# Performance work log

Hardware: AMD Instinct MI355X
Metric: run time of the kernel (lower is better)

Reference implementation:

```python
import jax, jax.numpy as jnp
import numpy as np

N = 50000          # num nodes
EPS = 1e-5         # BatchNorm eps


def _spmm(row, col, val, x):
    # sparse (COO) @ dense: out[r] += val_e * x[c] for each edge e=(r,c)
    return jax.ops.segment_sum(val[:, None] * x[col], row, num_segments=N)


def setup_inputs() -> dict:
    key = jax.random.key(0)
    ks = jax.random.split(key, 12)
    E1, E2 = 1_000_000, 2_000_000
    IN, H, OUT = 512, 64, 40
    return {
        "x": jax.random.normal(ks[0], (N, IN), jnp.float32),
        "adj_row": jax.random.randint(ks[1], (E1,), 0, N, jnp.int32),
        "adj_col": jax.random.randint(ks[2], (E1,), 0, N, jnp.int32),
        "adj_val": jax.random.uniform(ks[3], (E1,), jnp.float32),
        "adj2_row": jax.random.randint(ks[4], (E2,), 0, N, jnp.int32),
        "adj2_col": jax.random.randint(ks[5], (E2,), 0, N, jnp.int32),
        "adj2_val": jax.random.uniform(ks[6], (E2,), jnp.float32),
        "W_embed": jax.random.normal(ks[7], (IN, H), jnp.float32) * 0.05,
        "b_embed": jnp.zeros((H,), jnp.float32),
        "bn_gamma": jnp.ones((2 * H,), jnp.float32),
        "bn_beta": jnp.zeros((2 * H,), jnp.float32),
        "bn_mean": jax.random.normal(ks[8], (2 * H,), jnp.float32) * 0.1,
        "bn_var": jax.random.uniform(ks[9], (2 * H,), jnp.float32) + 0.5,
        "W_final": jax.random.normal(ks[10], (7 * H, OUT), jnp.float32) * 0.05,
        "b_final": jnp.zeros((OUT,), jnp.float32),
    }


def reference(x, adj_row, adj_col, adj_val, adj2_row, adj2_col, adj2_val,
              W_embed, b_embed, bn_gamma, bn_beta, bn_mean, bn_var,
              W_final, b_final):
    # feature embed (1-layer MLP) + relu
    h = jax.nn.relu(x @ W_embed + b_embed)                       # [N, H]
    xs = [h]
    # conv 1: two-hop aggregation + concat, then BatchNorm (eval mode)
    h1 = jnp.concatenate([_spmm(adj_row, adj_col, adj_val, h),
                          _spmm(adj2_row, adj2_col, adj2_val, h)], axis=1)  # [N, 2H]
    h1 = (h1 - bn_mean) * jax.lax.rsqrt(bn_var + EPS) * bn_gamma + bn_beta
    xs.append(h1)
    # conv 2 (last conv, no BN)
    h2 = jnp.concatenate([_spmm(adj_row, adj_col, adj_val, h1),
                          _spmm(adj2_row, adj2_col, adj2_val, h1)], axis=1)  # [N, 4H]
    xs.append(h2)
    # JumpingKnowledge cat -> [N, 7H], final projection
    jk = jnp.concatenate(xs, axis=1)
    return jk @ W_final + b_final                                # [N, OUT]
```

## Files before the change

kernel.cpp:

```cpp
#include <hip/hip_runtime.h>

#define BN_EPS 1e-5f
#define MAXBINS 128

typedef __attribute__((ext_vector_type(8))) short bf16x8;
typedef __attribute__((ext_vector_type(4))) float f32x4;

__device__ __forceinline__ ushort f2bf(float f) {
  uint u = __float_as_uint(f);
  u += 0x7fffu + ((u >> 16) & 1u);
  return (ushort)(u >> 16);
}
__device__ __forceinline__ float bf2f(ushort u) {
  return __uint_as_float((uint)u << 16);
}
__device__ __forceinline__ uint pack2bf(float a, float b) {
  return (uint)f2bf(a) | ((uint)f2bf(b) << 16);
}
__device__ __forceinline__ void fma8(float acc[8], uint4 wv, float v) {
  acc[0] += v * __uint_as_float(wv.x << 16);
  acc[1] += v * __uint_as_float(wv.x & 0xffff0000u);
  acc[2] += v * __uint_as_float(wv.y << 16);
  acc[3] += v * __uint_as_float(wv.y & 0xffff0000u);
  acc[4] += v * __uint_as_float(wv.z << 16);
  acc[5] += v * __uint_as_float(wv.z & 0xffff0000u);
  acc[6] += v * __uint_as_float(wv.w << 16);
  acc[7] += v * __uint_as_float(wv.w & 0xffff0000u);
}

__global__ __launch_bounds__(256) void prep_weights(
    const float* __restrict__ We, const float* __restrict__ Wf,
    ushort* __restrict__ Wet, ushort* __restrict__ Wtg) {
  int i = blockIdx.x * 256 + threadIdx.x;
  if (i < 32768) {
    int col = i >> 9, k = i & 511;
    Wet[(size_t)col * 512 + k] = f2bf(We[(size_t)k * 64 + col]);
  } else if (i < 32768 + 24576) {
    int j = i - 32768;
    int col = j / 192, k = j % 192;
    float v = 0.f;
    if (col < 40)       v = Wf[(size_t)k * 40 + col];
    else if (col < 80)  { if (k >= 64) v = Wf[(size_t)(128 + k) * 40 + (col - 40)]; }
    else if (col < 120) { if (k >= 64) v = Wf[(size_t)(256 + k) * 40 + (col - 80)]; }
    Wtg[(size_t)col * 192 + k] = f2bf(v);
  }
}

__global__ __launch_bounds__(256) void embed_mfma(
    const float* __restrict__ x, const ushort* __restrict__ Wet,
    const float* __restrict__ b, ushort* __restrict__ hb, int N) {
  const int tid  = threadIdx.x;
  const int wv   = tid >> 6;
  const int lane = tid & 63;
  const int m16  = lane & 15;
  const int kg   = lane >> 4;
  const int row0 = blockIdx.x * 128 + wv * 32;

  f32x4 acc[2][4];
#pragma unroll
  for (int i = 0; i < 2; ++i)
#pragma unroll
    for (int t = 0; t < 4; ++t) acc[i][t] = (f32x4){0.f, 0.f, 0.f, 0.f};

#pragma unroll 4
  for (int ks = 0; ks < 16; ++ks) {
    const int kk = ks * 32 + kg * 8;
    bf16x8 afr[2];
#pragma unroll
    for (int i = 0; i < 2; ++i) {
      int grow = row0 + i * 16 + m16;
      grow = (grow < N) ? grow : (N - 1);
      const float* ap = x + (size_t)grow * 512 + kk;
      float4 lo = *reinterpret_cast<const float4*>(ap);
      float4 hi = *reinterpret_cast<const float4*>(ap + 4);
      uint4 pk;
      pk.x = pack2bf(lo.x, lo.y); pk.y = pack2bf(lo.z, lo.w);
      pk.z = pack2bf(hi.x, hi.y); pk.w = pack2bf(hi.z, hi.w);
      afr[i] = *reinterpret_cast<const bf16x8*>(&pk);
    }
#pragma unroll
    for (int t = 0; t < 4; ++t) {
      bf16x8 bfr = *reinterpret_cast<const bf16x8*>(
          Wet + (size_t)(t * 16 + m16) * 512 + kk);
      acc[0][t] = __builtin_amdgcn_mfma_f32_16x16x32_bf16(afr[0], bfr, acc[0][t], 0, 0, 0);
      acc[1][t] = __builtin_amdgcn_mfma_f32_16x16x32_bf16(afr[1], bfr, acc[1][t], 0, 0, 0);
    }
  }

#pragma unroll
  for (int i = 0; i < 2; ++i) {
    const int rbase = row0 + i * 16 + kg * 4;
#pragma unroll
    for (int t = 0; t < 4; ++t) {
      const int col = t * 16 + m16;
      const float bias = b[col];
#pragma unroll
      for (int reg = 0; reg < 4; ++reg) {
        int gr = rbase + reg;
        if (gr < N)
          hb[(size_t)gr * 64 + col] = f2bf(fmaxf(acc[i][t][reg] + bias, 0.f));
      }
    }
  }
}

__global__ __launch_bounds__(256) void bin_hist(
    const int* __restrict__ rows, int* __restrict__ gbin, int E, int nbins) {
  __shared__ int lb[MAXBINS];
  const int tid = threadIdx.x;
  if (tid < nbins) lb[tid] = 0;
  __syncthreads();
  const int stride = gridDim.x * blockDim.x;
  for (int i = blockIdx.x * blockDim.x + tid; i < E; i += stride)
    atomicAdd(&lb[rows[i] >> 9], 1);
  __syncthreads();
  if (tid < nbins && lb[tid]) atomicAdd(&gbin[tid], lb[tid]);
}

__device__ __forceinline__ void scan_bins_dev(
    const int* gbin, int* gbase, int* gcur, int nbins, int lane) {
  int carry = 0;
  for (int ch = 0; ch * 64 < nbins; ++ch) {
    int idx = ch * 64 + lane;
    int v = (idx < nbins) ? gbin[idx] : 0;
    int inc = v;
#pragma unroll
    for (int off = 1; off < 64; off <<= 1) {
      int y = __shfl_up(inc, off);
      if (lane >= off) inc += y;
    }
    int ex = carry + inc - v;
    if (idx < nbins) { gbase[idx] = ex; gcur[idx] = ex; }
    carry += __shfl(inc, 63);
  }
}

__global__ __launch_bounds__(64) void bin_scan(
    const int* __restrict__ gbin1, int* __restrict__ gbase1, int* __restrict__ gcur1,
    const int* __restrict__ gbin2, int* __restrict__ gbase2, int* __restrict__ gcur2,
    int nbins) {
  int lane = threadIdx.x;
  scan_bins_dev(gbin1, gbase1, gcur1, nbins, lane);
  scan_bins_dev(gbin2, gbase2, gcur2, nbins, lane);
}

__global__ __launch_bounds__(256) void bin_scatter(
    const int* __restrict__ rows, const int* __restrict__ cols,
    const float* __restrict__ vals, int E, int* __restrict__ gcur,
    int2* __restrict__ S, int nbins) {
  __shared__ int lcnt[MAXBINS];
  __shared__ int lcur[MAXBINS];
  const int tid = threadIdx.x;
  for (int e0 = blockIdx.x * 2048; e0 < E; e0 += gridDim.x * 2048) {
    int i0 = e0 + tid * 8;
    int r[8], c[8], vb[8];
    if (i0 + 8 <= E) {
      int4 a = *reinterpret_cast<const int4*>(rows + i0);
      int4 b = *reinterpret_cast<const int4*>(rows + i0 + 4);
      r[0]=a.x; r[1]=a.y; r[2]=a.z; r[3]=a.w; r[4]=b.x; r[5]=b.y; r[6]=b.z; r[7]=b.w;
      a = *reinterpret_cast<const int4*>(cols + i0);
      b = *reinterpret_cast<const int4*>(cols + i0 + 4);
      c[0]=a.x; c[1]=a.y; c[2]=a.z; c[3]=a.w; c[4]=b.x; c[5]=b.y; c[6]=b.z; c[7]=b.w;
      a = *reinterpret_cast<const int4*>(vals + i0);
      b = *reinterpret_cast<const int4*>(vals + i0 + 4);
      vb[0]=a.x; vb[1]=a.y; vb[2]=a.z; vb[3]=a.w; vb[4]=b.x; vb[5]=b.y; vb[6]=b.z; vb[7]=b.w;
    } else {
#pragma unroll
      for (int t = 0; t < 8; ++t) {
        int i = i0 + t;
        bool ok = i < E;
        r[t]  = ok ? rows[i] : -1;
        c[t]  = ok ? cols[i] : 0;
        vb[t] = ok ? __float_as_int(vals[i]) : 0;
      }
    }
    if (tid < nbins) lcnt[tid] = 0;
    __syncthreads();
#pragma unroll
    for (int t = 0; t < 8; ++t)
      if (r[t] >= 0) atomicAdd(&lcnt[r[t] >> 9], 1);
    __syncthreads();
    if (tid < nbins) {
      int n = lcnt[tid];
      lcur[tid] = n ? atomicAdd(&gcur[tid], n) : 0;
    }
    __syncthreads();
#pragma unroll
    for (int t = 0; t < 8; ++t) {
      if (r[t] >= 0) {
        int pos = atomicAdd(&lcur[r[t] >> 9], 1);
        S[pos] = make_int2(c[t] | ((r[t] & 511) << 16), vb[t]);
      }
    }
    __syncthreads();
  }
}

__global__ __launch_bounds__(256) void csr_finalize(
    const int2* __restrict__ S1, const int* __restrict__ gbase1,
    int* __restrict__ rp1, uint* __restrict__ Eo1, int Etot1,
    const int2* __restrict__ S2, const int* __restrict__ gbase2,
    int* __restrict__ rp2, uint* __restrict__ Eo2, int Etot2,
    int N, int nbins) {
  __shared__ int cnt[512];
  __shared__ int cur[512];
  const int tid = threadIdx.x;
  const int b = blockIdx.x % nbins;
  const int g = blockIdx.x / nbins;
  const int2* S     = g ? S2 : S1;
  const int* gbase  = g ? gbase2 : gbase1;
  int* rp           = g ? rp2 : rp1;
  uint* Eo          = g ? Eo2 : Eo1;
  const int Etot    = g ? Etot2 : Etot1;

  const int base = gbase[b];
  const int end  = (b + 1 < nbins) ? gbase[b + 1] : Etot;
  const int r0   = b << 9;
  const int nrows = min(512, N - r0);

  for (int l = tid; l < 512; l += 256) cnt[l] = 0;
  __syncthreads();
  for (int j = base + tid; j < end; j += 256)
    atomicAdd(&cnt[S[j].x >> 16], 1);
  __syncthreads();
  if (tid < 64) {
    int carry = 0;
#pragma unroll
    for (int ch = 0; ch < 8; ++ch) {
      int v = cnt[ch * 64 + tid];
      int inc = v;
#pragma unroll
      for (int off = 1; off < 64; off <<= 1) {
        int y = __shfl_up(inc, off);
        if (tid >= off) inc += y;
      }
      inc += carry;
      cnt[ch * 64 + tid] = inc;
      carry = __shfl(inc, 63);
    }
  }
  __syncthreads();
  for (int l = tid; l < 512; l += 256)
    cur[l] = base + ((l > 0) ? cnt[l - 1] : 0);
  for (int l = tid; l < nrows; l += 256)
    rp[r0 + l + 1] = base + cnt[l];
  if (b == 0 && tid == 0) rp[0] = 0;
  __syncthreads();
  for (int j = base + tid; j < end; j += 256) {
    int2 m = S[j];
    int pos = atomicAdd(&cur[m.x >> 16], 1);
    Eo[pos] = (uint)(m.x & 0xffff) | ((uint)f2bf(__int_as_float(m.y)) << 16);
  }
}

__global__ __launch_bounds__(256) void conv1_gather(
    const ushort* __restrict__ hb,
    const int* __restrict__ rp1, const uint* __restrict__ E1,
    const int* __restrict__ rp2, const uint* __restrict__ E2,
    const float* __restrict__ gamma, const float* __restrict__ beta,
    const float* __restrict__ mean, const float* __restrict__ var,
    ushort* __restrict__ h1b, int N, int nwaves) {
  const int wid  = (blockIdx.x * blockDim.x + threadIdx.x) >> 6;
  const int lane = threadIdx.x & 63;
  const int sub  = lane >> 3;
  const int q    = lane & 7;

  float sc1[8], sh1[8], sc2[8], sh2[8];
#pragma unroll
  for (int t4 = 0; t4 < 2; ++t4) {
    int f1 = q * 8 + t4 * 4;
    float4 gm = *reinterpret_cast<const float4*>(gamma + f1);
    float4 vr = *reinterpret_cast<const float4*>(var + f1);
    float4 mn = *reinterpret_cast<const float4*>(mean + f1);
    float4 bt = *reinterpret_cast<const float4*>(beta + f1);
    float s0 = gm.x * rsqrtf(vr.x + BN_EPS), s1 = gm.y * rsqrtf(vr.y + BN_EPS);
    float s2 = gm.z * rsqrtf(vr.z + BN_EPS), s3 = gm.w * rsqrtf(vr.w + BN_EPS);
    sc1[t4 * 4 + 0] = s0; sh1[t4 * 4 + 0] = bt.x - mn.x * s0;
    sc1[t4 * 4 + 1] = s1; sh1[t4 * 4 + 1] = bt.y - mn.y * s1;
    sc1[t4 * 4 + 2] = s2; sh1[t4 * 4 + 2] = bt.z - mn.z * s2;
    sc1[t4 * 4 + 3] = s3; sh1[t4 * 4 + 3] = bt.w - mn.w * s3;
    int f2 = 64 + f1;
    gm = *reinterpret_cast<const float4*>(gamma + f2);
    vr = *reinterpret_cast<const float4*>(var + f2);
    mn = *reinterpret_cast<const float4*>(mean + f2);
    bt = *reinterpret_cast<const float4*>(beta + f2);
    s0 = gm.x * rsqrtf(vr.x + BN_EPS); s1 = gm.y * rsqrtf(vr.y + BN_EPS);
    s2 = gm.z * rsqrtf(vr.z + BN_EPS); s3 = gm.w * rsqrtf(vr.w + BN_EPS);
    sc2[t4 * 4 + 0] = s0; sh2[t4 * 4 + 0] = bt.x - mn.x * s0;
    sc2[t4 * 4 + 1] = s1; sh2[t4 * 4 + 1] = bt.y - mn.y * s1;
    sc2[t4 * 4 + 2] = s2; sh2[t4 * 4 + 2] = bt.z - mn.z * s2;
    sc2[t4 * 4 + 3] = s3; sh2[t4 * 4 + 3] = bt.w - mn.w * s3;
  }

  for (int r = wid; r < N; r += nwaves) {
    float acc1[8] = {0, 0, 0, 0, 0, 0, 0, 0};
    float acc2[8] = {0, 0, 0, 0, 0, 0, 0, 0};
    {
      int s = rp1[r], e = rp1[r + 1];
      for (int j0 = s; j0 < e; j0 += 32) {
        int j = j0 + sub;
        uint m0 = (j      < e) ? E1[j]      : 0u;
        uint m1 = (j + 8  < e) ? E1[j + 8]  : 0u;
        uint m2 = (j + 16 < e) ? E1[j + 16] : 0u;
        uint m3 = (j + 24 < e) ? E1[j + 24] : 0u;
        uint4 w0 = *reinterpret_cast<const uint4*>(hb + (size_t)(m0 & 0xffffu) * 64 + q * 8);
        uint4 w1 = *reinterpret_cast<const uint4*>(hb + (size_t)(m1 & 0xffffu) * 64 + q * 8);
        uint4 w2 = *reinterpret_cast<const uint4*>(hb + (size_t)(m2 & 0xffffu) * 64 + q * 8);
        uint4 w3 = *reinterpret_cast<const uint4*>(hb + (size_t)(m3 & 0xffffu) * 64 + q * 8);
        fma8(acc1, w0, bf2f((ushort)(m0 >> 16)));
        fma8(acc1, w1, bf2f((ushort)(m1 >> 16)));
        fma8(acc1, w2, bf2f((ushort)(m2 >> 16)));
        fma8(acc1, w3, bf2f((ushort)(m3 >> 16)));
      }
    }
    {
      int s = rp2[r], e = rp2[r + 1];
      for (int j0 = s; j0 < e; j0 += 32) {
        int j = j0 + sub;
        uint m0 = (j      < e) ? E2[j]      : 0u;
        uint m1 = (j + 8  < e) ? E2[j + 8]  : 0u;
        uint m2 = (j + 16 < e) ? E2[j + 16] : 0u;
        uint m3 = (j + 24 < e) ? E2[j + 24] : 0u;
        uint4 w0 = *reinterpret_cast<const uint4*>(hb + (size_t)(m0 & 0xffffu) * 64 + q * 8);
        uint4 w1 = *reinterpret_cast<const uint4*>(hb + (size_t)(m1 & 0xffffu) * 64 + q * 8);
        uint4 w2 = *reinterpret_cast<const uint4*>(hb + (size_t)(m2 & 0xffffu) * 64 + q * 8);
        uint4 w3 = *reinterpret_cast<const uint4*>(hb + (size_t)(m3 & 0xffffu) * 64 + q * 8);
        fma8(acc2, w0, bf2f((ushort)(m0 >> 16)));
        fma8(acc2, w1, bf2f((ushort)(m1 >> 16)));
        fma8(acc2, w2, bf2f((ushort)(m2 >> 16)));
        fma8(acc2, w3, bf2f((ushort)(m3 >> 16)));
      }
    }
#pragma unroll
    for (int mask = 8; mask <= 32; mask <<= 1) {
#pragma unroll
      for (int t = 0; t < 8; ++t) {
        acc1[t] += __shfl_xor(acc1[t], mask);
        acc2[t] += __shfl_xor(acc2[t], mask);
      }
    }
    if (lane < 8) {
      uint4 p1, p2;
      p1.x = pack2bf(acc1[0] * sc1[0] + sh1[0], acc1[1] * sc1[1] + sh1[1]);
      p1.y = pack2bf(acc1[2] * sc1[2] + sh1[2], acc1[3] * sc1[3] + sh1[3]);
      p1.z = pack2bf(acc1[4] * sc1[4] + sh1[4], acc1[5] * sc1[5] + sh1[5]);
      p1.w = pack2bf(acc1[6] * sc1[6] + sh1[6], acc1[7] * sc1[7] + sh1[7]);
      p2.x = pack2bf(acc2[0] * sc2[0] + sh2[0], acc2[1] * sc2[1] + sh2[1]);
      p2.y = pack2bf(acc2[2] * sc2[2] + sh2[2], acc2[3] * sc2[3] + sh2[3]);
      p2.z = pack2bf(acc2[4] * sc2[4] + sh2[4], acc2[5] * sc2[5] + sh2[5]);
      p2.w = pack2bf(acc2[6] * sc2[6] + sh2[6], acc2[7] * sc2[7] + sh2[7]);
      ushort* dst = h1b + (size_t)r * 128 + q * 8;
      *reinterpret_cast<uint4*>(dst)      = p1;
      *reinterpret_cast<uint4*>(dst + 64) = p2;
    }
  }
}

__global__ __launch_bounds__(256) void dense_tail_mfma(
    const ushort* __restrict__ hb, const ushort* __restrict__ h1b,
    const ushort* __restrict__ Wtg, const float* __restrict__ bfin,
    float* __restrict__ out, ushort* __restrict__ g1b, ushort* __restrict__ g2b,
    int N) {
  const int tid  = threadIdx.x;
  const int wv   = tid >> 6;
  const int lane = tid & 63;
  const int m16  = lane & 15;
  const int kg   = lane >> 4;
  const int row0 = blockIdx.x * 128;

  f32x4 acc[2][8];
#pragma unroll
  for (int i = 0; i < 2; ++i)
#pragma unroll
    for (int t = 0; t < 8; ++t) acc[i][t] = (f32x4){0.f, 0.f, 0.f, 0.f};

#pragma unroll
  for (int ks = 0; ks < 6; ++ks) {
    const int kk = ks * 32 + kg * 8;
    bf16x8 afr[2];
#pragma unroll
    for (int i = 0; i < 2; ++i) {
      int grow = row0 + wv * 32 + i * 16 + m16;
      grow = (grow < N) ? grow : (N - 1);
      const ushort* ap = (kk < 64) ? hb + (size_t)grow * 64 + kk
                                   : h1b + (size_t)grow * 128 + (kk - 64);
      afr[i] = *reinterpret_cast<const bf16x8*>(ap);
    }
#pragma unroll
    for (int t = 0; t < 8; ++t) {
      bf16x8 bfr = *reinterpret_cast<const bf16x8*>(
          Wtg + (size_t)(t * 16 + m16) * 192 + kk);
      acc[0][t] = __builtin_amdgcn_mfma_f32_16x16x32_bf16(afr[0], bfr, acc[0][t], 0, 0, 0);
      acc[1][t] = __builtin_amdgcn_mfma_f32_16x16x32_bf16(afr[1], bfr, acc[1][t], 0, 0, 0);
    }
  }

#pragma unroll
  for (int i = 0; i < 2; ++i) {
    const int rbase = row0 + wv * 32 + i * 16 + kg * 4;
#pragma unroll
    for (int t = 0; t < 8; ++t) {
      const int col = t * 16 + m16;
      if (col >= 120) continue;
      const float bias = (col < 40) ? bfin[col] : 0.f;
#pragma unroll
      for (int reg = 0; reg < 4; ++reg) {
        int gr = rbase + reg;
        if (gr < N) {
          float v = acc[i][t][reg];
          if (col < 40)       out[(size_t)gr * 40 + col] = v + bias;
          else if (col < 80)  g1b[(size_t)gr * 40 + (col - 40)] = f2bf(v);
          else                g2b[(size_t)gr * 40 + (col - 80)] = f2bf(v);
        }
      }
    }
  }
}

__global__ __launch_bounds__(256) void final_add_kernel(
    const ushort* __restrict__ g1b, const ushort* __restrict__ g2b,
    const int* __restrict__ rp1, const uint* __restrict__ E1,
    const int* __restrict__ rp2, const uint* __restrict__ E2,
    float* __restrict__ out, int N, int nwaves) {
  const int wid  = (blockIdx.x * blockDim.x + threadIdx.x) >> 6;
  const int lane = threadIdx.x & 63;
  const int sub  = lane >> 3;
  const int q    = lane & 7;
  const int off  = (q < 5) ? q * 8 : 0;

  for (int r = wid; r < N; r += nwaves) {
    float a1[8] = {0, 0, 0, 0, 0, 0, 0, 0};
    float a2[8] = {0, 0, 0, 0, 0, 0, 0, 0};
    {
      int s = rp1[r], e = rp1[r + 1];
      for (int j0 = s; j0 < e; j0 += 32) {
        int j = j0 + sub;
        uint m0 = (j      < e) ? E1[j]      : 0u;
        uint m1 = (j + 8  < e) ? E1[j + 8]  : 0u;
        uint m2 = (j + 16 < e) ? E1[j + 16] : 0u;
        uint m3 = (j + 24 < e) ? E1[j + 24] : 0u;
        uint4 w0 = *reinterpret_cast<const uint4*>(g1b + (size_t)(m0 & 0xffffu) * 40 + off);
        uint4 w1 = *reinterpret_cast<const uint4*>(g1b + (size_t)(m1 & 0xffffu) * 40 + off);
        uint4 w2 = *reinterpret_cast<const uint4*>(g1b + (size_t)(m2 & 0xffffu) * 40 + off);
        uint4 w3 = *reinterpret_cast<const uint4*>(g1b + (size_t)(m3 & 0xffffu) * 40 + off);
        fma8(a1, w0, bf2f((ushort)(m0 >> 16)));
        fma8(a1, w1, bf2f((ushort)(m1 >> 16)));
        fma8(a1, w2, bf2f((ushort)(m2 >> 16)));
        fma8(a1, w3, bf2f((ushort)(m3 >> 16)));
      }
    }
    {
      int s = rp2[r], e = rp2[r + 1];
      for (int j0 = s; j0 < e; j0 += 32) {
        int j = j0 + sub;
        uint m0 = (j      < e) ? E2[j]      : 0u;
        uint m1 = (j + 8  < e) ? E2[j + 8]  : 0u;
        uint m2 = (j + 16 < e) ? E2[j + 16] : 0u;
        uint m3 = (j + 24 < e) ? E2[j + 24] : 0u;
        uint4 w0 = *reinterpret_cast<const uint4*>(g2b + (size_t)(m0 & 0xffffu) * 40 + off);
        uint4 w1 = *reinterpret_cast<const uint4*>(g2b + (size_t)(m1 & 0xffffu) * 40 + off);
        uint4 w2 = *reinterpret_cast<const uint4*>(g2b + (size_t)(m2 & 0xffffu) * 40 + off);
        uint4 w3 = *reinterpret_cast<const uint4*>(g2b + (size_t)(m3 & 0xffffu) * 40 + off);
        fma8(a2, w0, bf2f((ushort)(m0 >> 16)));
        fma8(a2, w1, bf2f((ushort)(m1 >> 16)));
        fma8(a2, w2, bf2f((ushort)(m2 >> 16)));
        fma8(a2, w3, bf2f((ushort)(m3 >> 16)));
      }
    }
#pragma unroll
    for (int mask = 8; mask <= 32; mask <<= 1) {
#pragma unroll
      for (int t = 0; t < 8; ++t) {
        a1[t] += __shfl_xor(a1[t], mask);
        a2[t] += __shfl_xor(a2[t], mask);
      }
    }
    if (lane < 5) {
      float* p = out + (size_t)r * 40 + lane * 8;
      float4 o0 = *reinterpret_cast<const float4*>(p);
      float4 o1 = *reinterpret_cast<const float4*>(p + 4);
      o0.x += a1[0] + a2[0]; o0.y += a1[1] + a2[1];
      o0.z += a1[2] + a2[2]; o0.w += a1[3] + a2[3];
      o1.x += a1[4] + a2[4]; o1.y += a1[5] + a2[5];
      o1.z += a1[6] + a2[6]; o1.w += a1[7] + a2[7];
      *reinterpret_cast<float4*>(p)     = o0;
      *reinterpret_cast<float4*>(p + 4) = o1;
    }
  }
}

extern "C" void kernel_launch(void* const* d_in, const int* in_sizes, int n_in,
                              void* d_out, int out_size, void* d_ws, size_t ws_size,
                              hipStream_t stream) {
  const float* x     = (const float*)d_in[0];
  const int*   a1r   = (const int*)d_in[1];
  const int*   a1c   = (const int*)d_in[2];
  const float* a1v   = (const float*)d_in[3];
  const int*   a2r   = (const int*)d_in[4];
  const int*   a2c   = (const int*)d_in[5];
  const float* a2v   = (const float*)d_in[6];
  const float* We    = (const float*)d_in[7];
  const float* be    = (const float*)d_in[8];
  const float* gamma = (const float*)d_in[9];
  const float* beta  = (const float*)d_in[10];
  const float* mean  = (const float*)d_in[11];
  const float* var   = (const float*)d_in[12];
  const float* Wf    = (const float*)d_in[13];
  const float* bf    = (const float*)d_in[14];
  float* out = (float*)d_out;

  const int N  = in_sizes[0] / 512;
  const int E1 = in_sizes[1];
  const int E2 = in_sizes[4];
  const int nbins = (N + 511) >> 9;

  char* p = (char*)d_ws;
  auto alloc = [&](size_t bytes) {
    char* q = p; p += (bytes + 255) & ~(size_t)255; return q;
  };
  ushort* hb   = (ushort*)alloc((size_t)N * 64 * 2);
  ushort* h1b  = (ushort*)alloc((size_t)N * 128 * 2);
  ushort* g1b  = (ushort*)alloc((size_t)N * 40 * 2);
  ushort* g2b  = (ushort*)alloc((size_t)N * 40 * 2);
  ushort* Wet  = (ushort*)alloc((size_t)64 * 512 * 2);
  ushort* Wtg  = (ushort*)alloc((size_t)128 * 192 * 2);
  int*    rp1  = (int*)   alloc(((size_t)N + 1) * 4);
  int*    rp2  = (int*)   alloc(((size_t)N + 1) * 4);
  uint*   E1s  = (uint*)  alloc((size_t)E1 * 4);
  uint*   E2s  = (uint*)  alloc((size_t)E2 * 4);
  int2*   S1   = (int2*)  alloc((size_t)E1 * 8);
  int2*   S2   = (int2*)  alloc((size_t)E2 * 8);
  int*    gbin1  = (int*) alloc(MAXBINS * 4);
  int*    gbin2  = (int*) alloc(MAXBINS * 4);
  int*    gbase1 = (int*) alloc(MAXBINS * 4);
  int*    gbase2 = (int*) alloc(MAXBINS * 4);
  int*    gcur1  = (int*) alloc(MAXBINS * 4);
  int*    gcur2  = (int*) alloc(MAXBINS * 4);

  hipMemsetAsync(gbin1, 0, (size_t)2 * MAXBINS * 4 + 256, stream);

  prep_weights<<<(32768 + 24576 + 255) / 256, 256, 0, stream>>>(We, Wf, Wet, Wtg);

  embed_mfma<<<(N + 127) / 128, 256, 0, stream>>>(x, Wet, be, hb, N);

  bin_hist<<<256, 256, 0, stream>>>(a1r, gbin1, E1, nbins);
  bin_hist<<<256, 256, 0, stream>>>(a2r, gbin2, E2, nbins);
  bin_scan<<<1, 64, 0, stream>>>(gbin1, gbase1, gcur1, gbin2, gbase2, gcur2, nbins);
  bin_scatter<<<256, 256, 0, stream>>>(a1r, a1c, a1v, E1, gcur1, S1, nbins);
  bin_scatter<<<256, 256, 0, stream>>>(a2r, a2c, a2v, E2, gcur2, S2, nbins);
  csr_finalize<<<2 * nbins, 256, 0, stream>>>(
      S1, gbase1, rp1, E1s, E1, S2, gbase2, rp2, E2s, E2, N, nbins);

  const int NW = 2048 * 4;
  conv1_gather<<<2048, 256, 0, stream>>>(
      hb, rp1, E1s, rp2, E2s, gamma, beta, mean, var, h1b, N, NW);

  dense_tail_mfma<<<(N + 127) / 128, 256, 0, stream>>>(
      hb, h1b, Wtg, bf, out, g1b, g2b, N);

  final_add_kernel<<<2048, 256, 0, stream>>>(
      g1b, g2b, rp1, E1s, rp2, E2s, out, N, NW);
}
```

Measured before the change: 303.6 us.

## Split gathered feature tables into column halves for cache-resident gathers

The 64-wide embedding table is split into two 32-column bf16 arrays, and conv1 runs two passes, one over each half. This shrinks the randomly gathered working set per pass (about 3.2MB instead of 6.4MB) so it fits better in cache. The 40-wide g1/g2 tables are likewise split into 32+8 column arrays, and final_add uses a full-wave gather for the 8-column tail. BatchNorm scale and shift are now computed once in prep_weights. The cost is that the edge lists and row pointers are read twice in conv1 and final_add, with more shuffle reductions and more passes.

```diff
diff --git a/kernel.cpp b/kernel.cpp
--- a/kernel.cpp
+++ b/kernel.cpp
@@ -30,7 +30,10 @@
 
 __global__ __launch_bounds__(256) void prep_weights(
     const float* __restrict__ We, const float* __restrict__ Wf,
-    ushort* __restrict__ Wet, ushort* __restrict__ Wtg) {
+    const float* __restrict__ gamma, const float* __restrict__ beta,
+    const float* __restrict__ mean, const float* __restrict__ var,
+    ushort* __restrict__ Wet, ushort* __restrict__ Wtg,
+    float* __restrict__ bnsc, float* __restrict__ bnsh) {
   int i = blockIdx.x * 256 + threadIdx.x;
   if (i < 32768) {
     int col = i >> 9, k = i & 511;
@@ -43,12 +46,18 @@
     else if (col < 80)  { if (k >= 64) v = Wf[(size_t)(128 + k) * 40 + (col - 40)]; }
     else if (col < 120) { if (k >= 64) v = Wf[(size_t)(256 + k) * 40 + (col - 80)]; }
     Wtg[(size_t)col * 192 + k] = f2bf(v);
+  } else if (i < 32768 + 24576 + 128) {
+    int c = i - 32768 - 24576;
+    float s = gamma[c] * rsqrtf(var[c] + BN_EPS);
+    bnsc[c] = s;
+    bnsh[c] = beta[c] - mean[c] * s;
   }
 }
 
 __global__ __launch_bounds__(256) void embed_mfma(
     const float* __restrict__ x, const ushort* __restrict__ Wet,
-    const float* __restrict__ b, ushort* __restrict__ hb, int N) {
+    const float* __restrict__ b, ushort* __restrict__ hbA,
+    ushort* __restrict__ hbB, int N) {
   const int tid  = threadIdx.x;
   const int wv   = tid >> 6;
   const int lane = tid & 63;
@@ -97,8 +106,11 @@
 #pragma unroll
       for (int reg = 0; reg < 4; ++reg) {
         int gr = rbase + reg;
-        if (gr < N)
-          hb[(size_t)gr * 64 + col] = f2bf(fmaxf(acc[i][t][reg] + bias, 0.f));
+        if (gr < N) {
+          ushort v = f2bf(fmaxf(acc[i][t][reg] + bias, 0.f));
+          if (col < 32) hbA[(size_t)gr * 32 + col] = v;
+          else          hbB[(size_t)gr * 32 + (col - 32)] = v;
+        }
       }
     }
   }
@@ -254,113 +266,84 @@
 }
 
 __global__ __launch_bounds__(256) void conv1_gather(
-    const ushort* __restrict__ hb,
+    const ushort* __restrict__ hbA, const ushort* __restrict__ hbB,
     const int* __restrict__ rp1, const uint* __restrict__ E1,
     const int* __restrict__ rp2, const uint* __restrict__ E2,
-    const float* __restrict__ gamma, const float* __restrict__ beta,
-    const float* __restrict__ mean, const float* __restrict__ var,
+    const float* __restrict__ bnsc, const float* __restrict__ bnsh,
     ushort* __restrict__ h1b, int N, int nwaves) {
   const int wid  = (blockIdx.x * blockDim.x + threadIdx.x) >> 6;
   const int lane = threadIdx.x & 63;
-  const int sub  = lane >> 3;
-  const int q    = lane & 7;
-
-  float sc1[8], sh1[8], sc2[8], sh2[8];
-#pragma unroll
-  for (int t4 = 0; t4 < 2; ++t4) {
-    int f1 = q * 8 + t4 * 4;
-    float4 gm = *reinterpret_cast<const float4*>(gamma + f1);
-    float4 vr = *reinterpret_cast<const float4*>(var + f1);
-    float4 mn = *reinterpret_cast<const float4*>(mean + f1);
-    float4 bt = *reinterpret_cast<const float4*>(beta + f1);
-    float s0 = gm.x * rsqrtf(vr.x + BN_EPS), s1 = gm.y * rsqrtf(vr.y + BN_EPS);
-    float s2 = gm.z * rsqrtf(vr.z + BN_EPS), s3 = gm.w * rsqrtf(vr.w + BN_EPS);
-    sc1[t4 * 4 + 0] = s0; sh1[t4 * 4 + 0] = bt.x - mn.x * s0;
-    sc1[t4 * 4 + 1] = s1; sh1[t4 * 4 + 1] = bt.y - mn.y * s1;
-    sc1[t4 * 4 + 2] = s2; sh1[t4 * 4 + 2] = bt.z - mn.z * s2;
-    sc1[t4 * 4 + 3] = s3; sh1[t4 * 4 + 3] = bt.w - mn.w * s3;
-    int f2 = 64 + f1;
-    gm = *reinterpret_cast<const float4*>(gamma + f2);
-    vr = *reinterpret_cast<const float4*>(var + f2);
-    mn = *reinterpret_cast<const float4*>(mean + f2);
-    bt = *reinterpret_cast<const float4*>(beta + f2);
-    s0 = gm.x * rsqrtf(vr.x + BN_EPS); s1 = gm.y * rsqrtf(vr.y + BN_EPS);
-    s2 = gm.z * rsqrtf(vr.z + BN_EPS); s3 = gm.w * rsqrtf(vr.w + BN_EPS);
-    sc2[t4 * 4 + 0] = s0; sh2[t4 * 4 + 0] = bt.x - mn.x * s0;
-    sc2[t4 * 4 + 1] = s1; sh2[t4 * 4 + 1] = bt.y - mn.y * s1;
-    sc2[t4 * 4 + 2] = s2; sh2[t4 * 4 + 2] = bt.z - mn.z * s2;
-    sc2[t4 * 4 + 3] = s3; sh2[t4 * 4 + 3] = bt.w - mn.w * s3;
-  }
+  const int sub  = lane >> 2;
+  const int q    = lane & 3;
 
   for (int r = wid; r < N; r += nwaves) {
-    float acc1[8] = {0, 0, 0, 0, 0, 0, 0, 0};
-    float acc2[8] = {0, 0, 0, 0, 0, 0, 0, 0};
-    {
-      int s = rp1[r], e = rp1[r + 1];
-      for (int j0 = s; j0 < e; j0 += 32) {
+    const int s1 = rp1[r], e1 = rp1[r + 1];
+    const int s2 = rp2[r], e2 = rp2[r + 1];
+#pragma unroll
+    for (int p = 0; p < 2; ++p) {
+      const ushort* src = p ? hbB : hbA;
+      float acc1[8] = {0, 0, 0, 0, 0, 0, 0, 0};
+      float acc2[8] = {0, 0, 0, 0, 0, 0, 0, 0};
+      for (int j0 = s1; j0 < e1; j0 += 32) {
         int j = j0 + sub;
-        uint m0 = (j      < e) ? E1[j]      : 0u;
-        uint m1 = (j + 8  < e) ? E1[j + 8]  : 0u;
-        uint m2 = (j + 16 < e) ? E1[j + 16] : 0u;
-        uint m3 = (j + 24 < e) ? E1[j + 24] : 0u;
-        uint4 w0 = *reinterpret_cast<const uint4*>(hb + (size_t)(m0 & 0xffffu) * 64 + q * 8);
-        uint4 w1 = *reinterpret_cast<const uint4*>(hb + (size_t)(m1 & 0xffffu) * 64 + q * 8);
-        uint4 w2 = *reinterpret_cast<const uint4*>(hb + (size_t)(m2 & 0xffffu) * 64 + q * 8);
-        uint4 w3 = *reinterpret_cast<const uint4*>(hb + (size_t)(m3 & 0xffffu) * 64 + q * 8);
-        fma8(acc1, w0, bf2f((ushort)(m0 >> 16)));
-        fma8(acc1, w1, bf2f((ushort)(m1 >> 16)));
-        fma8(acc1, w2, bf2f((ushort)(m2 >> 16)));
-        fma8(acc1, w3, bf2f((ushort)(m3 >> 16)));
-      }
-    }
-    {
-      int s = rp2[r], e = rp2[r + 1];
-      for (int j0 = s; j0 < e; j0 += 32) {
+        uint m0 = (j      < e1) ? E1[j]      : 0u;
+        uint m1 = (j + 16 < e1) ? E1[j + 16] : 0u;
+        uint4 w0 = *reinterpret_cast<const uint4*>(src + (size_t)(m0 & 0xffffu) * 32 + q * 8);
+        uint4 w1 = *reinterpret_cast<const uint4*>(src + (size_t)(m1 & 0xffffu) * 32 + q * 8);
+        fma8(acc1, w0, __uint_as_float(m0 & 0xffff0000u));
+        fma8(acc1, w1, __uint_as_float(m1 & 0xffff0000u));
+      }
+      for (int j0 = s2; j0 < e2; j0 += 32) {
         int j = j0 + sub;
-        uint m0 = (j      < e) ? E2[j]      : 0u;
-        uint m1 = (j + 8  < e) ? E2[j + 8]  : 0u;
-        uint m2 = (j + 16 < e) ? E2[j + 16] : 0u;
-        uint m3 = (j + 24 < e) ? E2[j + 24] : 0u;
-        uint4 w0 = *reinterpret_cast<const uint4*>(hb + (size_t)(m0 & 0xffffu) * 64 + q * 8);
-        uint4 w1 = *reinterpret_cast<const uint4*>(hb + (size_t)(m1 & 0xffffu) * 64 + q * 8);
-        uint4 w2 = *reinterpret_cast<const uint4*>(hb + (size_t)(m2 & 0xffffu) * 64 + q * 8);
-        uint4 w3 = *reinterpret_cast<const uint4*>(hb + (size_t)(m3 & 0xffffu) * 64 + q * 8);
-        fma8(acc2, w0, bf2f((ushort)(m0 >> 16)));
-        fma8(acc2, w1, bf2f((ushort)(m1 >> 16)));
-        fma8(acc2, w2, bf2f((ushort)(m2 >> 16)));
-        fma8(acc2, w3, bf2f((ushort)(m3 >> 16)));
-      }
-    }
-#pragma unroll
-    for (int mask = 8; mask <= 32; mask <<= 1) {
-#pragma unroll
-      for (int t = 0; t < 8; ++t) {
-        acc1[t] += __shfl_xor(acc1[t], mask);
-        acc2[t] += __shfl_xor(acc2[t], mask);
-      }
-    }
-    if (lane < 8) {
-      uint4 p1, p2;
-      p1.x = pack2bf(acc1[0] * sc1[0] + sh1[0], acc1[1] * sc1[1] + sh1[1]);
-      p1.y = pack2bf(acc1[2] * sc1[2] + sh1[2], acc1[3] * sc1[3] + sh1[3]);
-      p1.z = pack2bf(acc1[4] * sc1[4] + sh1[4], acc1[5] * sc1[5] + sh1[5]);
-      p1.w = pack2bf(acc1[6] * sc1[6] + sh1[6], acc1[7] * sc1[7] + sh1[7]);
-      p2.x = pack2bf(acc2[0] * sc2[0] + sh2[0], acc2[1] * sc2[1] + sh2[1]);
-      p2.y = pack2bf(acc2[2] * sc2[2] + sh2[2], acc2[3] * sc2[3] + sh2[3]);
-      p2.z = pack2bf(acc2[4] * sc2[4] + sh2[4], acc2[5] * sc2[5] + sh2[5]);
-      p2.w = pack2bf(acc2[6] * sc2[6] + sh2[6], acc2[7] * sc2[7] + sh2[7]);
-      ushort* dst = h1b + (size_t)r * 128 + q * 8;
-      *reinterpret_cast<uint4*>(dst)      = p1;
-      *reinterpret_cast<uint4*>(dst + 64) = p2;
+        uint m0 = (j      < e2) ? E2[j]      : 0u;
+        uint m1 = (j + 16 < e2) ? E2[j + 16] : 0u;
+        uint4 w0 = *reinterpret_cast<const uint4*>(src + (size_t)(m0 & 0xffffu) * 32 + q * 8);
+        uint4 w1 = *reinterpret_cast<const uint4*>(src + (size_t)(m1 & 0xffffu) * 32 + q * 8);
+        fma8(acc2, w0, __uint_as_float(m0 & 0xffff0000u));
+        fma8(acc2, w1, __uint_as_float(m1 & 0xffff0000u));
+      }
+#pragma unroll
+      for (int mask = 4; mask <= 32; mask <<= 1) {
+#pragma unroll
+        for (int t = 0; t < 8; ++t) {
+          acc1[t] += __shfl_xor(acc1[t], mask);
+          acc2[t] += __shfl_xor(acc2[t], mask);
+        }
+      }
+      if (lane < 4) {
+        const int f = p * 32 + q * 8;
+        float4 scA0 = *reinterpret_cast<const float4*>(bnsc + f);
+        float4 scA1 = *reinterpret_cast<const float4*>(bnsc + f + 4);
+        float4 shA0 = *reinterpret_cast<const float4*>(bnsh + f);
+        float4 shA1 = *reinterpret_cast<const float4*>(bnsh + f + 4);
+        float4 scB0 = *reinterpret_cast<const float4*>(bnsc + 64 + f);
+        float4 scB1 = *reinterpret_cast<const float4*>(bnsc + 64 + f + 4);
+        float4 shB0 = *reinterpret_cast<const float4*>(bnsh + 64 + f);
+        float4 shB1 = *reinterpret_cast<const float4*>(bnsh + 64 + f + 4);
+        uint4 p1, p2;
+        p1.x = pack2bf(acc1[0] * scA0.x + shA0.x, acc1[1] * scA0.y + shA0.y);
+        p1.y = pack2bf(acc1[2] * scA0.z + shA0.z, acc1[3] * scA0.w + shA0.w);
+        p1.z = pack2bf(acc1[4] * scA1.x + shA1.x, acc1[5] * scA1.y + shA1.y);
+        p1.w = pack2bf(acc1[6] * scA1.z + shA1.z, acc1[7] * scA1.w + shA1.w);
+        p2.x = pack2bf(acc2[0] * scB0.x + shB0.x, acc2[1] * scB0.y + shB0.y);
+        p2.y = pack2bf(acc2[2] * scB0.z + shB0.z, acc2[3] * scB0.w + shB0.w);
+        p2.z = pack2bf(acc2[4] * scB1.x + shB1.x, acc2[5] * scB1.y + shB1.y);
+        p2.w = pack2bf(acc2[6] * scB1.z + shB1.z, acc2[7] * scB1.w + shB1.w);
+        ushort* dst = h1b + (size_t)r * 128 + p * 32 + q * 8;
+        *reinterpret_cast<uint4*>(dst)      = p1;
+        *reinterpret_cast<uint4*>(dst + 64) = p2;
+      }
     }
   }
 }
 
 __global__ __launch_bounds__(256) void dense_tail_mfma(
-    const ushort* __restrict__ hb, const ushort* __restrict__ h1b,
+    const ushort* __restrict__ hbA, const ushort* __restrict__ hbB,
+    const ushort* __restrict__ h1b,
     const ushort* __restrict__ Wtg, const float* __restrict__ bfin,
-    float* __restrict__ out, ushort* __restrict__ g1b, ushort* __restrict__ g2b,
-    int N) {
+    float* __restrict__ out,
+    ushort* __restrict__ g1A, ushort* __restrict__ g1B,
+    ushort* __restrict__ g2A, ushort* __restrict__ g2B, int N) {
   const int tid  = threadIdx.x;
   const int wv   = tid >> 6;
   const int lane = tid & 63;
@@ -382,8 +365,10 @@
     for (int i = 0; i < 2; ++i) {
       int grow = row0 + wv * 32 + i * 16 + m16;
       grow = (grow < N) ? grow : (N - 1);
-      const ushort* ap = (kk < 64) ? hb + (size_t)grow * 64 + kk
-                                   : h1b + (size_t)grow * 128 + (kk - 64);
+      const ushort* ap;
+      if (ks == 0)      ap = hbA + (size_t)grow * 32 + kk;
+      else if (ks == 1) ap = hbB + (size_t)grow * 32 + (kk - 32);
+      else              ap = h1b + (size_t)grow * 128 + (kk - 64);
       afr[i] = *reinterpret_cast<const bf16x8*>(ap);
     }
 #pragma unroll
@@ -408,9 +393,17 @@
         int gr = rbase + reg;
         if (gr < N) {
           float v = acc[i][t][reg];
-          if (col < 40)       out[(size_t)gr * 40 + col] = v + bias;
-          else if (col < 80)  g1b[(size_t)gr * 40 + (col - 40)] = f2bf(v);
-          else                g2b[(size_t)gr * 40 + (col - 80)] = f2bf(v);
+          if (col < 40) {
+            out[(size_t)gr * 40 + col] = v + bias;
+          } else if (col < 80) {
+            int f = col - 40;
+            if (f < 32) g1A[(size_t)gr * 32 + f] = f2bf(v);
+            else        g1B[(size_t)gr * 8 + (f - 32)] = f2bf(v);
+          } else {
+            int f = col - 80;
+            if (f < 32) g2A[(size_t)gr * 32 + f] = f2bf(v);
+            else        g2B[(size_t)gr * 8 + (f - 32)] = f2bf(v);
+          }
         }
       }
     }
@@ -418,71 +411,77 @@
 }
 
 __global__ __launch_bounds__(256) void final_add_kernel(
-    const ushort* __restrict__ g1b, const ushort* __restrict__ g2b,
+    const ushort* __restrict__ g1A, const ushort* __restrict__ g1B,
+    const ushort* __restrict__ g2A, const ushort* __restrict__ g2B,
     const int* __restrict__ rp1, const uint* __restrict__ E1,
     const int* __restrict__ rp2, const uint* __restrict__ E2,
     float* __restrict__ out, int N, int nwaves) {
   const int wid  = (blockIdx.x * blockDim.x + threadIdx.x) >> 6;
   const int lane = threadIdx.x & 63;
-  const int sub  = lane >> 3;
-  const int q    = lane & 7;
-  const int off  = (q < 5) ? q * 8 : 0;
+  const int sub  = lane >> 2;
+  const int q    = lane & 3;
 
   for (int r = wid; r < N; r += nwaves) {
-    float a1[8] = {0, 0, 0, 0, 0, 0, 0, 0};
-    float a2[8] = {0, 0, 0, 0, 0, 0, 0, 0};
-    {
-      int s = rp1[r], e = rp1[r + 1];
-      for (int j0 = s; j0 < e; j0 += 32) {
-        int j = j0 + sub;
-        uint m0 = (j      < e) ? E1[j]      : 0u;
-        uint m1 = (j + 8  < e) ? E1[j + 8]  : 0u;
-        uint m2 = (j + 16 < e) ? E1[j + 16] : 0u;
-        uint m3 = (j + 24 < e) ? E1[j + 24] : 0u;
-        uint4 w0 = *reinterpret_cast<const uint4*>(g1b + (size_t)(m0 & 0xffffu) * 40 + off);
-        uint4 w1 = *reinterpret_cast<const uint4*>(g1b + (size_t)(m1 & 0xffffu) * 40 + off);
-        uint4 w2 = *reinterpret_cast<const uint4*>(g1b + (size_t)(m2 & 0xffffu) * 40 + off);
-        uint4 w3 = *reinterpret_cast<const uint4*>(g1b + (size_t)(m3 & 0xffffu) * 40 + off);
-        fma8(a1, w0, bf2f((ushort)(m0 >> 16)));
-        fma8(a1, w1, bf2f((ushort)(m1 >> 16)));
-        fma8(a1, w2, bf2f((ushort)(m2 >> 16)));
-        fma8(a1, w3, bf2f((ushort)(m3 >> 16)));
-      }
-    }
-    {
-      int s = rp2[r], e = rp2[r + 1];
-      for (int j0 = s; j0 < e; j0 += 32) {
-        int j = j0 + sub;
-        uint m0 = (j      < e) ? E2[j]      : 0u;
-        uint m1 = (j + 8  < e) ? E2[j + 8]  : 0u;
-        uint m2 = (j + 16 < e) ? E2[j + 16] : 0u;
-        uint m3 = (j + 24 < e) ? E2[j + 24] : 0u;
-        uint4 w0 = *reinterpret_cast<const uint4*>(g2b + (size_t)(m0 & 0xffffu) * 40 + off);
-        uint4 w1 = *reinterpret_cast<const uint4*>(g2b + (size_t)(m1 & 0xffffu) * 40 + off);
-        uint4 w2 = *reinterpret_cast<const uint4*>(g2b + (size_t)(m2 & 0xffffu) * 40 + off);
-        uint4 w3 = *reinterpret_cast<const uint4*>(g2b + (size_t)(m3 & 0xffffu) * 40 + off);
-        fma8(a2, w0, bf2f((ushort)(m0 >> 16)));
-        fma8(a2, w1, bf2f((ushort)(m1 >> 16)));
-        fma8(a2, w2, bf2f((ushort)(m2 >> 16)));
-        fma8(a2, w3, bf2f((ushort)(m3 >> 16)));
-      }
-    }
-#pragma unroll
-    for (int mask = 8; mask <= 32; mask <<= 1) {
-#pragma unroll
-      for (int t = 0; t < 8; ++t) {
-        a1[t] += __shfl_xor(a1[t], mask);
-        a2[t] += __shfl_xor(a2[t], mask);
-      }
-    }
-    if (lane < 5) {
-      float* p = out + (size_t)r * 40 + lane * 8;
+    const int s1 = rp1[r], e1 = rp1[r + 1];
+    const int s2 = rp2[r], e2 = rp2[r + 1];
+
+    float a[8] = {0, 0, 0, 0, 0, 0, 0, 0};
+    for (int j0 = s1; j0 < e1; j0 += 32) {
+      int j = j0 + sub;
+      uint m0 = (j      < e1) ? E1[j]      : 0u;
+      uint m1 = (j + 16 < e1) ? E1[j + 16] : 0u;
+      uint4 w0 = *reinterpret_cast<const uint4*>(g1A + (size_t)(m0 & 0xffffu) * 32 + q * 8);
+      uint4 w1 = *reinterpret_cast<const uint4*>(g1A + (size_t)(m1 & 0xffffu) * 32 + q * 8);
+      fma8(a, w0, __uint_as_float(m0 & 0xffff0000u));
+      fma8(a, w1, __uint_as_float(m1 & 0xffff0000u));
+    }
+    for (int j0 = s2; j0 < e2; j0 += 32) {
+      int j = j0 + sub;
+      uint m0 = (j      < e2) ? E2[j]      : 0u;
+      uint m1 = (j + 16 < e2) ? E2[j + 16] : 0u;
+      uint4 w0 = *reinterpret_cast<const uint4*>(g2A + (size_t)(m0 & 0xffffu) * 32 + q * 8);
+      uint4 w1 = *reinterpret_cast<const uint4*>(g2A + (size_t)(m1 & 0xffffu) * 32 + q * 8);
+      fma8(a, w0, __uint_as_float(m0 & 0xffff0000u));
+      fma8(a, w1, __uint_as_float(m1 & 0xffff0000u));
+    }
+#pragma unroll
+    for (int mask = 4; mask <= 32; mask <<= 1)
+#pragma unroll
+      for (int t = 0; t < 8; ++t) a[t] += __shfl_xor(a[t], mask);
+
+    float bb[8] = {0, 0, 0, 0, 0, 0, 0, 0};
+    for (int j0 = s1; j0 < e1; j0 += 64) {
+      int j = j0 + lane;
+      uint m = (j < e1) ? E1[j] : 0u;
+      uint4 w = *reinterpret_cast<const uint4*>(g1B + (size_t)(m & 0xffffu) * 8);
+      fma8(bb, w, __uint_as_float(m & 0xffff0000u));
+    }
+    for (int j0 = s2; j0 < e2; j0 += 64) {
+      int j = j0 + lane;
+      uint m = (j < e2) ? E2[j] : 0u;
+      uint4 w = *reinterpret_cast<const uint4*>(g2B + (size_t)(m & 0xffffu) * 8);
+      fma8(bb, w, __uint_as_float(m & 0xffff0000u));
+    }
+#pragma unroll
+    for (int mask = 1; mask <= 32; mask <<= 1)
+#pragma unroll
+      for (int t = 0; t < 8; ++t) bb[t] += __shfl_xor(bb[t], mask);
+
+    if (lane < 4) {
+      float* p = out + (size_t)r * 40 + q * 8;
       float4 o0 = *reinterpret_cast<const float4*>(p);
       float4 o1 = *reinterpret_cast<const float4*>(p + 4);
-      o0.x += a1[0] + a2[0]; o0.y += a1[1] + a2[1];
-      o0.z += a1[2] + a2[2]; o0.w += a1[3] + a2[3];
-      o1.x += a1[4] + a2[4]; o1.y += a1[5] + a2[5];
-      o1.z += a1[6] + a2[6]; o1.w += a1[7] + a2[7];
+      o0.x += a[0]; o0.y += a[1]; o0.z += a[2]; o0.w += a[3];
+      o1.x += a[4]; o1.y += a[5]; o1.z += a[6]; o1.w += a[7];
+      *reinterpret_cast<float4*>(p)     = o0;
+      *reinterpret_cast<float4*>(p + 4) = o1;
+    }
+    if (lane == 0) {
+      float* p = out + (size_t)r * 40 + 32;
+      float4 o0 = *reinterpret_cast<const float4*>(p);
+      float4 o1 = *reinterpret_cast<const float4*>(p + 4);
+      o0.x += bb[0]; o0.y += bb[1]; o0.z += bb[2]; o0.w += bb[3];
+      o1.x += bb[4]; o1.y += bb[5]; o1.z += bb[6]; o1.w += bb[7];
       *reinterpret_cast<float4*>(p)     = o0;
       *reinterpret_cast<float4*>(p + 4) = o1;
     }
@@ -518,12 +517,17 @@
   auto alloc = [&](size_t bytes) {
     char* q = p; p += (bytes + 255) & ~(size_t)255; return q;
   };
-  ushort* hb   = (ushort*)alloc((size_t)N * 64 * 2);
+  ushort* hbA  = (ushort*)alloc((size_t)N * 32 * 2);
+  ushort* hbB  = (ushort*)alloc((size_t)N * 32 * 2);
   ushort* h1b  = (ushort*)alloc((size_t)N * 128 * 2);
-  ushort* g1b  = (ushort*)alloc((size_t)N * 40 * 2);
-  ushort* g2b  = (ushort*)alloc((size_t)N * 40 * 2);
+  ushort* g1A  = (ushort*)alloc((size_t)N * 32 * 2);
+  ushort* g1B  = (ushort*)alloc((size_t)N * 8 * 2);
+  ushort* g2A  = (ushort*)alloc((size_t)N * 32 * 2);
+  ushort* g2B  = (ushort*)alloc((size_t)N * 8 * 2);
   ushort* Wet  = (ushort*)alloc((size_t)64 * 512 * 2);
   ushort* Wtg  = (ushort*)alloc((size_t)128 * 192 * 2);
+  float*  bnsc = (float*) alloc(128 * 4);
+  float*  bnsh = (float*) alloc(128 * 4);
   int*    rp1  = (int*)   alloc(((size_t)N + 1) * 4);
   int*    rp2  = (int*)   alloc(((size_t)N + 1) * 4);
   uint*   E1s  = (uint*)  alloc((size_t)E1 * 4);
@@ -539,9 +543,10 @@
 
   hipMemsetAsync(gbin1, 0, (size_t)2 * MAXBINS * 4 + 256, stream);
 
-  prep_weights<<<(32768 + 24576 + 255) / 256, 256, 0, stream>>>(We, Wf, Wet, Wtg);
-
-  embed_mfma<<<(N + 127) / 128, 256, 0, stream>>>(x, Wet, be, hb, N);
+  prep_weights<<<(32768 + 24576 + 128 + 255) / 256, 256, 0, stream>>>(
+      We, Wf, gamma, beta, mean, var, Wet, Wtg, bnsc, bnsh);
+
+  embed_mfma<<<(N + 127) / 128, 256, 0, stream>>>(x, Wet, be, hbA, hbB, N);
 
   bin_hist<<<256, 256, 0, stream>>>(a1r, gbin1, E1, nbins);
   bin_hist<<<256, 256, 0, stream>>>(a2r, gbin2, E2, nbins);
@@ -553,11 +558,11 @@
 
   const int NW = 2048 * 4;
   conv1_gather<<<2048, 256, 0, stream>>>(
-      hb, rp1, E1s, rp2, E2s, gamma, beta, mean, var, h1b, N, NW);
+      hbA, hbB, rp1, E1s, rp2, E2s, bnsc, bnsh, h1b, N, NW);
 
   dense_tail_mfma<<<(N + 127) / 128, 256, 0, stream>>>(
-      hb, h1b, Wtg, bf, out, g1b, g2b, N);
+      hbA, hbB, h1b, Wtg, bf, out, g1A, g1B, g2A, g2B, N);
 
   final_add_kernel<<<2048, 256, 0, stream>>>(
-      g1b, g2b, rp1, E1s, rp2, E2s, out, N, NW);
-}
+      g1A, g1B, g2A, g2B, rp1, E1s, rp2, E2s, out, N, NW);
+}
```

Measured after the change: 346.5 us. +14.1%, slower.
